# Kernel optimization log

Measured on AMD Instinct MI355X. Metric: run time of the kernel, lower is better.

## Reference

```python
import jax, jax.numpy as jnp
import numpy as np
import math

B, H, W = 4, 256, 256
S = 256          # num_superpixels
ZD = 128         # z_dim
GC = 256         # g_channels
NBLK = 8


def setup_inputs() -> dict:
    key = jax.random.key(0)
    ks = jax.random.split(key, 12)
    rn = lambda k, shp, s=1.0: jax.random.normal(k, shp, jnp.float32) * s
    return {
        "z": rn(ks[0], (B, ZD)),
        "images": rn(ks[1], (B, 3, H, W)),
        "segments": jax.random.randint(ks[2], (B, H, W), 0, S).astype(jnp.int32),
        # row-stochastic-ish adjacency scale keeps 8 propagations stable
        "A": rn(ks[3], (B, S, S), 1.0 / math.sqrt(S)),
        # WSConv2d weights: init N(0,1); forward multiplies input by sqrt(2/(in*k*k))
        "proj_w": rn(ks[4], (GC, 3 + ZD)), "proj_b": jnp.zeros((GC,), jnp.float32),
        "blk_proj_w": rn(ks[5], (NBLK, GC, GC)), "blk_proj_b": jnp.zeros((NBLK, GC), jnp.float32),
        "ada1_w": rn(ks[6], (NBLK, 2 * GC, GC)), "ada1_b": jnp.zeros((NBLK, 2 * GC), jnp.float32),
        "ada2_w": rn(ks[7], (NBLK, 2 * GC, 2 * GC)), "ada2_b": jnp.zeros((NBLK, 2 * GC), jnp.float32),
        # plain Conv2d 3x3 layers in upsample head
        "up1_w": rn(ks[8], (GC // 2, GC, 3, 3), 0.02), "up1_b": jnp.zeros((GC // 2,), jnp.float32),
        "up2_w": rn(ks[9], (3, GC // 2, 3, 3), 0.02), "up2_b": jnp.zeros((3,), jnp.float32),
    }


def _ws1x1(x, w, b):
    # WSConv2d with 1x1 kernel over node dim: x [B,Cin,S] -> [B,Cout,S]
    scale = math.sqrt(2.0 / w.shape[1])
    return jnp.einsum('oc,bcs->bos', w, x) * scale + b[None, :, None]


def _conv3(x, w, b):
    y = jax.lax.conv_general_dilated(x, w, (1, 1), 'SAME',
                                     dimension_numbers=('NCHW', 'OIHW', 'NCHW'))
    return y + b[None, :, None, None]


def _forward(z, images, A, proj_w, proj_b, blk_proj_w, blk_proj_b,
             ada1_w, ada1_b, ada2_w, ada2_b, up1_w, up1_b, up2_w, up2_b,
             segments):
    Bn, _, Hn, Wn = images.shape
    N = Hn * Wn
    flat = images.reshape(Bn, 3, N)            # [B,3,N]
    seg = segments.reshape(Bn, N)              # [B,N] int

    # superpixel mean pooling (math of one_hot^T @ flat / counts, as segment-sum)
    seg_sum = jax.vmap(lambda f, s: jax.ops.segment_sum(f, s, num_segments=S))(
        flat.transpose(0, 2, 1), seg)          # [B,S,3]
    counts = jax.vmap(lambda s: jax.ops.segment_sum(
        jnp.ones(s.shape, jnp.float32), s, num_segments=S))(seg)  # [B,S]
    feats = seg_sum / (counts[..., None] + 1e-6)

    z_rep = jnp.broadcast_to(z[:, None, :], (Bn, S, ZD))
    x = jnp.concatenate([feats, z_rep], axis=2).transpose(0, 2, 1)  # [B,3+ZD,S]
    x = _ws1x1(x, proj_w, proj_b)                                   # [B,GC,S]

    for i in range(NBLK):
        h = _ws1x1(x, blk_proj_w[i], blk_proj_b[i])
        # A @ feat : out[b,c,i] = sum_j A[b,i,j] h[b,c,j]
        h = jnp.einsum('bij,bcj->bci', A, h)
        # AdaIN: style from global mean over nodes
        m = h.mean(axis=2, keepdims=True)                    # [B,GC,1]
        s1 = jax.nn.leaky_relu(_ws1x1(m, ada1_w[i], ada1_b[i]), 0.2)
        style = _ws1x1(s1, ada2_w[i], ada2_b[i])             # [B,2GC,1]
        gamma, beta = jnp.split(style, 2, axis=1)
        h = gamma * h + beta
        x = jax.nn.leaky_relu(h, 0.2)                        # dropout=0 (eval)

    # broadcast superpixel feats back to pixels (math of one_hot @ sup_feats)
    sup_feats = x.transpose(0, 2, 1)                         # [B,S,GC]
    pix = jnp.take_along_axis(sup_feats, seg[:, :, None].astype(jnp.int32), axis=1)  # [B,N,GC]
    pix = pix.transpose(0, 2, 1).reshape(Bn, GC, Hn, Wn)

    y = jax.nn.leaky_relu(_conv3(pix, up1_w, up1_b), 0.2)
    y = _conv3(y, up2_w, up2_b)                              # [B,3,H,W]
    # InstanceNorm2d(3), affine=False, eps=1e-5
    mu = y.mean((2, 3), keepdims=True)
    var = y.var((2, 3), keepdims=True)
    y = (y - mu) / jnp.sqrt(var + 1e-5)
    return jnp.tanh(y)


def reference(z, images, segments, A, proj_w, proj_b, blk_proj_w, blk_proj_b,
              ada1_w, ada1_b, ada2_w, ada2_b, up1_w, up1_b, up2_w, up2_b):
    return _forward(z, images, A, proj_w, proj_b, blk_proj_w, blk_proj_b,
                    ada1_w, ada1_b, ada2_w, ada2_b, up1_w, up1_b, up2_w, up2_b,
                    segments)
```

## Files before the change

### kernel.cpp

```cpp
#include <hip/hip_runtime.h>
#include <cmath>

#define BB 4
#define SS 256
#define ZDIM 128
#define GCH 256
#define NBLKS 8
#define NPIX 65536
#define U1C 128

__device__ __forceinline__ float lrelu(float x){ return x >= 0.f ? x : 0.2f*x; }

__global__ __launch_bounds__(256) void k_pp(const float* __restrict__ img,
        const int* __restrict__ seg, float* __restrict__ segsum,
        float* __restrict__ counts, const float* __restrict__ A,
        const float* __restrict__ w1, const float* __restrict__ w2,
        float* __restrict__ At2, float* __restrict__ wT, float* __restrict__ w2t){
  int bid = blockIdx.x;
  int tid = threadIdx.x;
  if(bid < 256){
    __shared__ float ls[SS*4];
    for(int j=tid;j<SS*4;j+=256) ls[j]=0.f;
    __syncthreads();
    int b = bid >> 6;
    int base = bid*1024;
    for(int it=0; it<4; it++){
      int idx = base + it*256 + tid;
      int n = idx & (NPIX-1);
      int s = seg[idx];
      atomicAdd(&ls[s*4+0], img[(b*3+0)*NPIX+n]);
      atomicAdd(&ls[s*4+1], img[(b*3+1)*NPIX+n]);
      atomicAdd(&ls[s*4+2], img[(b*3+2)*NPIX+n]);
      atomicAdd(&ls[s*4+3], 1.0f);
    }
    __syncthreads();
    for(int j=tid;j<SS*4;j+=256){
      int s = j>>2, c = j&3;
      float vv = ls[j];
      if(vv != 0.f){
        if(c<3) atomicAdd(&segsum[(b*SS+s)*3+c], vv);
        else    atomicAdd(&counts[b*SS+s], vv);
      }
    }
  } else if(bid < 512){
    __shared__ float t[32][33];
    int sb = bid - 256;
    int b = sb >> 6;
    int bx = (sb & 7)*32, by = ((sb >> 3) & 7)*32;
    int lx = tid & 31, ly4 = (tid >> 5)*4;
    #pragma unroll
    for(int r=0;r<4;r++)
      t[ly4+r][lx] = A[(b<<16) + ((by+ly4+r)<<8) + bx + lx];
    __syncthreads();
    #pragma unroll
    for(int r=0;r<4;r++){
      int jj = bx + ly4 + r;
      int i  = by + lx;
      At2[(b<<16) + ((jj>>2)<<10) + (i<<2) + (jj&3)] = t[lx][ly4+r];
    }
  } else {
    int idx = (bid-512)*256 + tid;
    if(idx < 294912){
      int o = idx & 127; int r = idx >> 7; int c = r & 255; int k = r >> 8;
      wT[idx] = w1[(o*GCH + c)*9 + k];
    } else if(idx < 294912 + 3456){
      int t2 = idx - 294912;
      int cc = t2 & 7;
      int oc = (t2 >> 3) % 3;
      int sg = (t2 / 24) & 3;
      int g  = (t2 / 96) & 3;
      int k  = t2 / 384;
      w2t[t2] = w2[oc*1152 + (g*32 + sg*8 + cc)*9 + k];
    }
  }
}

__global__ __launch_bounds__(256) void k_x0(const float* __restrict__ segsum,
        const float* __restrict__ counts, const float* __restrict__ z,
        const float* __restrict__ pw, const float* __restrict__ pb,
        float sc, float4* __restrict__ xp2){
  int og = blockIdx.x;
  int b  = blockIdx.y;
  int i  = threadIdx.x;
  float cnt = counts[b*SS+i] + 1e-6f;
  float f0 = segsum[(b*SS+i)*3+0]/cnt;
  float f1 = segsum[(b*SS+i)*3+1]/cnt;
  float f2 = segsum[(b*SS+i)*3+2]/cnt;
  const float* zb = z + b*ZDIM;
  float vals[4];
  #pragma unroll
  for(int oo=0;oo<4;oo++){
    int o = og*4 + oo;
    const float* wr = pw + o*131;
    float acc = wr[0]*f0 + wr[1]*f1 + wr[2]*f2;
    #pragma unroll 8
    for(int j=0;j<ZDIM;j++) acc += wr[3+j]*zb[j];
    vals[oo] = acc*sc + pb[o];
  }
  float4 o4 = {vals[0], vals[1], vals[2], vals[3]};
  xp2[(b*64+og)*256 + i] = o4;
}

__global__ __launch_bounds__(512) void k_gemm(const float4* __restrict__ xp2,
        const float* __restrict__ bw, const float* __restrict__ bb,
        const float4* __restrict__ At2, float sc,
        float* __restrict__ h2, float* __restrict__ m){
  int c0 = blockIdx.x*4;
  int b  = blockIdx.y;
  int tid = threadIdx.x;
  int j  = tid & 255;
  int h  = tid >> 8;
  __shared__ float4 wl4[4][64];
  __shared__ float ps[8][260];
  __shared__ float4 h1l4[4][66];
  __shared__ float red[4][4];
  for(int t = tid; t < 1024; t += 512){
    int row = t >> 8, jj = t & 255;
    ((float*)&wl4[row][0])[jj] = bw[(c0+row)*GCH + jj];
  }
  __syncthreads();
  {
    const float4* xb = xp2 + (b*64 + h*32)*256 + j;
    float a0=0.f, a1=0.f, a2=0.f, a3=0.f;
    #pragma unroll 8
    for(int kg=0; kg<32; kg++){
      float4 x  = xb[kg*256];
      float4 w0 = wl4[0][h*32+kg];
      float4 w1v= wl4[1][h*32+kg];
      float4 w2v= wl4[2][h*32+kg];
      float4 w3 = wl4[3][h*32+kg];
      a0 += w0.x*x.x + w0.y*x.y + w0.z*x.z + w0.w*x.w;
      a1 += w1v.x*x.x + w1v.y*x.y + w1v.z*x.z + w1v.w*x.w;
      a2 += w2v.x*x.x + w2v.y*x.y + w2v.z*x.z + w2v.w*x.w;
      a3 += w3.x*x.x + w3.y*x.y + w3.z*x.z + w3.w*x.w;
    }
    ps[0+h][j] = a0; ps[2+h][j] = a1; ps[4+h][j] = a2; ps[6+h][j] = a3;
  }
  __syncthreads();
  if(tid < 256){
    #pragma unroll
    for(int ch=0;ch<4;ch++){
      float vv = (ps[ch*2][tid] + ps[ch*2+1][tid])*sc + bb[c0+ch];
      ((float*)&h1l4[ch][0])[tid] = vv;
    }
  }
  __syncthreads();
  {
    const float4* ab = At2 + (b*64 + h*32)*256 + j;
    float r0=0.f, r1=0.f, r2=0.f, r3=0.f;
    #pragma unroll 8
    for(int kg=0; kg<32; kg++){
      float4 a  = ab[kg*256];
      float4 h0 = h1l4[0][h*32+kg];
      float4 h1 = h1l4[1][h*32+kg];
      float4 h2v= h1l4[2][h*32+kg];
      float4 h3 = h1l4[3][h*32+kg];
      r0 += a.x*h0.x + a.y*h0.y + a.z*h0.z + a.w*h0.w;
      r1 += a.x*h1.x + a.y*h1.y + a.z*h1.z + a.w*h1.w;
      r2 += a.x*h2v.x + a.y*h2v.y + a.z*h2v.z + a.w*h2v.w;
      r3 += a.x*h3.x + a.y*h3.y + a.z*h3.z + a.w*h3.w;
    }
    ps[0+h][j] = r0; ps[2+h][j] = r1; ps[4+h][j] = r2; ps[6+h][j] = r3;
  }
  __syncthreads();
  float rr0=0.f, rr1=0.f, rr2=0.f, rr3=0.f;
  if(tid < 256){
    rr0 = ps[0][tid]+ps[1][tid];
    rr1 = ps[2][tid]+ps[3][tid];
    rr2 = ps[4][tid]+ps[5][tid];
    rr3 = ps[6][tid]+ps[7][tid];
    h2[(b*GCH+c0+0)*SS + tid] = rr0;
    h2[(b*GCH+c0+1)*SS + tid] = rr1;
    h2[(b*GCH+c0+2)*SS + tid] = rr2;
    h2[(b*GCH+c0+3)*SS + tid] = rr3;
  }
  for(int off=32; off; off>>=1){
    rr0 += __shfl_down(rr0,off); rr1 += __shfl_down(rr1,off);
    rr2 += __shfl_down(rr2,off); rr3 += __shfl_down(rr3,off);
  }
  if(tid < 256 && (tid & 63)==0){
    int w3 = tid >> 6;
    red[0][w3]=rr0; red[1][w3]=rr1; red[2][w3]=rr2; red[3][w3]=rr3;
  }
  __syncthreads();
  if(tid < 4)
    m[b*GCH + c0 + tid] =
      (red[tid][0]+red[tid][1]+red[tid][2]+red[tid][3])*(1.f/256.f);
}

__global__ __launch_bounds__(512) void k_s12(const float* __restrict__ m,
        const float* __restrict__ a1w, const float* __restrict__ a1b,
        const float* __restrict__ a2w, const float* __restrict__ a2b,
        const float* __restrict__ h2, float sc1, float sc2,
        float4* __restrict__ xp2){
  int q = blockIdx.x;
  int tid = threadIdx.x;
  int lane = tid & 63, wv = tid >> 6;
  int grp = lane >> 3, ll = lane & 7;
  __shared__ float4 ml4[256];
  __shared__ float s1l[4][512];
  __shared__ float gbl[4][16];
  if(tid < 256) ml4[tid] = ((const float4*)m)[tid];
  __syncthreads();
  #pragma unroll 2
  for(int pass=0; pass<8; pass++){
    int row = wv*64 + pass*8 + grp;
    const float4* ar = (const float4*)(a1w + row*GCH) + ll;
    float p0=0.f,p1=0.f,p2=0.f,p3=0.f;
    #pragma unroll
    for(int j=0;j<8;j++){
      float4 w4 = ar[j*8];
      float4 m0 = ml4[0*64 + j*8 + ll];
      float4 m1 = ml4[1*64 + j*8 + ll];
      float4 m2 = ml4[2*64 + j*8 + ll];
      float4 m3 = ml4[3*64 + j*8 + ll];
      p0 += w4.x*m0.x + w4.y*m0.y + w4.z*m0.z + w4.w*m0.w;
      p1 += w4.x*m1.x + w4.y*m1.y + w4.z*m1.z + w4.w*m1.w;
      p2 += w4.x*m2.x + w4.y*m2.y + w4.z*m2.z + w4.w*m2.w;
      p3 += w4.x*m3.x + w4.y*m3.y + w4.z*m3.z + w4.w*m3.w;
    }
    #pragma unroll
    for(int off=1; off<8; off<<=1){
      p0 += __shfl_xor(p0,off); p1 += __shfl_xor(p1,off);
      p2 += __shfl_xor(p2,off); p3 += __shfl_xor(p3,off);
    }
    if(ll == 0){
      float bv = a1b[row];
      int sidx = ((row & 7) << 6) + (row >> 3);
      s1l[0][sidx] = lrelu(p0*sc1 + bv);
      s1l[1][sidx] = lrelu(p1*sc1 + bv);
      s1l[2][sidx] = lrelu(p2*sc1 + bv);
      s1l[3][sidx] = lrelu(p3*sc1 + bv);
    }
  }
  __syncthreads();
  float sA[4][8];
  #pragma unroll
  for(int b=0;b<4;b++)
    #pragma unroll
    for(int j=0;j<8;j++) sA[b][j] = s1l[b][j*64 + lane];
  #pragma unroll
  for(int r=0;r<2;r++){
    int ridx = wv*2 + r;
    int cc = ridx & 7;
    int t = (ridx < 8) ? (q*8 + cc) : (256 + q*8 + cc);
    const float* wr = a2w + t*512 + lane*8;
    float4 wa = *(const float4*)wr;
    float4 wb4 = *(const float4*)(wr+4);
    float p0 = wa.x*sA[0][0]+wa.y*sA[0][1]+wa.z*sA[0][2]+wa.w*sA[0][3]
             + wb4.x*sA[0][4]+wb4.y*sA[0][5]+wb4.z*sA[0][6]+wb4.w*sA[0][7];
    float p1 = wa.x*sA[1][0]+wa.y*sA[1][1]+wa.z*sA[1][2]+wa.w*sA[1][3]
             + wb4.x*sA[1][4]+wb4.y*sA[1][5]+wb4.z*sA[1][6]+wb4.w*sA[1][7];
    float p2 = wa.x*sA[2][0]+wa.y*sA[2][1]+wa.z*sA[2][2]+wa.w*sA[2][3]
             + wb4.x*sA[2][4]+wb4.y*sA[2][5]+wb4.z*sA[2][6]+wb4.w*sA[2][7];
    float p3 = wa.x*sA[3][0]+wa.y*sA[3][1]+wa.z*sA[3][2]+wa.w*sA[3][3]
             + wb4.x*sA[3][4]+wb4.y*sA[3][5]+wb4.z*sA[3][6]+wb4.w*sA[3][7];
    for(int off=32; off; off>>=1){
      p0 += __shfl_xor(p0,off); p1 += __shfl_xor(p1,off);
      p2 += __shfl_xor(p2,off); p3 += __shfl_xor(p3,off);
    }
    if(lane < 4){
      float p = lane==0 ? p0 : lane==1 ? p1 : lane==2 ? p2 : p3;
      gbl[lane][ridx] = p*sc2 + a2b[t];
    }
  }
  __syncthreads();
  int j = tid & 255;
  int cg2 = tid >> 8;
  int cbase = q*8 + cg2*4;
  int cg = cbase >> 2;
  #pragma unroll
  for(int b=0;b<4;b++){
    float4 o;
    o.x = lrelu(gbl[b][cg2*4+0]*h2[(b*GCH + cbase+0)*SS + j] + gbl[b][8+cg2*4+0]);
    o.y = lrelu(gbl[b][cg2*4+1]*h2[(b*GCH + cbase+1)*SS + j] + gbl[b][8+cg2*4+1]);
    o.z = lrelu(gbl[b][cg2*4+2]*h2[(b*GCH + cbase+2)*SS + j] + gbl[b][8+cg2*4+2]);
    o.w = lrelu(gbl[b][cg2*4+3]*h2[(b*GCH + cbase+3)*SS + j] + gbl[b][8+cg2*4+3]);
    xp2[(b*64 + cg)*256 + j] = o;
  }
}

__global__ __launch_bounds__(256) void k_v(const float4* __restrict__ xp2,
        const float4* __restrict__ wT4, float4* __restrict__ v4){
  int s0 = blockIdx.x*16;
  int k  = blockIdx.y;
  int b  = blockIdx.z;
  int tid = threadIdx.x;
  __shared__ float4 wl[64][33];
  __shared__ float xft[256][17];
  for(int t = tid; t < 1024; t += 256){
    int cg = t >> 4, si = t & 15;
    float4 xv = xp2[(b*64 + cg)*256 + s0 + si];
    xft[cg*4+0][si] = xv.x;
    xft[cg*4+1][si] = xv.y;
    xft[cg*4+2][si] = xv.z;
    xft[cg*4+3][si] = xv.w;
  }
  int og = tid & 31, sh = tid >> 5;
  const float4* wb = wT4 + (size_t)k*GCH*32;
  float4 a0 = {0.f,0.f,0.f,0.f}, a1 = {0.f,0.f,0.f,0.f};
  for(int ct=0; ct<4; ct++){
    __syncthreads();
    for(int t = tid; t < 2048; t += 256){
      int cc = t>>5, o = t&31;
      wl[cc][o] = wb[(ct*64+cc)*32 + o];
    }
    __syncthreads();
    #pragma unroll 4
    for(int cc=0;cc<64;cc++){
      float4 w = wl[cc][og];
      int c = ct*64+cc;
      float x0v = xft[c][sh];
      float x1v = xft[c][8+sh];
      a0.x += w.x*x0v; a0.y += w.y*x0v; a0.z += w.z*x0v; a0.w += w.w*x0v;
      a1.x += w.x*x1v; a1.y += w.y*x1v; a1.z += w.z*x1v; a1.w += w.w*x1v;
    }
  }
  size_t base = (size_t)(b*9+k)*SS + s0;
  v4[(base + sh)*32 + og]     = a0;
  v4[(base + 8 + sh)*32 + og] = a1;
}

__global__ __launch_bounds__(256) void k_conv(const float4* __restrict__ v4,
        const int* __restrict__ seg, const float4* __restrict__ b14,
        const float* __restrict__ w2t, float* __restrict__ y2){
  __shared__ float4 y1t4[100*9];
  __shared__ int   segl[144];
  __shared__ float part[768];
  int bid = blockIdx.x;
  int x = bid & 7;
  int b = x >> 1;
  int sub = ((bid >> 3) << 1) + (x & 1);
  int g = sub & 3;
  int tile = sub >> 2;
  int x0p = (tile & 31)*8, y0p = (tile >> 5)*8;
  int tid = threadIdx.x;
  if(tid < 144){
    int r = tid/12, cc = tid%12;
    int gy = y0p - 2 + r, gx = x0p - 2 + cc;
    segl[tid] = (gy>=0 && gy<256 && gx>=0 && gx<256) ? seg[(b*256+gy)*256+gx] : -1;
  }
  __syncthreads();
  int o2 = tid & 3;
  const float4* vb = v4 + (size_t)(b*9)*SS*32 + g*8 + o2*2;
  float4 biasA = b14[g*8 + o2*2];
  float4 biasB = b14[g*8 + o2*2 + 1];
  bool interior = (x0p >= 8 && x0p <= 240 && y0p >= 8 && y0p <= 240);
  if(interior){
    for(int task = tid; task < 400; task += 256){
      int pp = task >> 2;
      int py = pp/10, px = pp - py*10;
      float4 aA = biasA, aB = biasB;
      #pragma unroll
      for(int k=0;k<9;k++){
        int sidx = segl[(py + k/3)*12 + (px + k%3)];
        const float4* pv = vb + (k*SS + sidx)*32;
        float4 vA = pv[0], vB = pv[1];
        aA.x += vA.x; aA.y += vA.y; aA.z += vA.z; aA.w += vA.w;
        aB.x += vB.x; aB.y += vB.y; aB.z += vB.z; aB.w += vB.w;
      }
      float4 valA, valB;
      valA.x = lrelu(aA.x); valA.y = lrelu(aA.y); valA.z = lrelu(aA.z); valA.w = lrelu(aA.w);
      valB.x = lrelu(aB.x); valB.y = lrelu(aB.y); valB.z = lrelu(aB.z); valB.w = lrelu(aB.w);
      y1t4[pp*9 + o2*2]     = valA;
      y1t4[pp*9 + o2*2 + 1] = valB;
    }
  } else {
    for(int task = tid; task < 400; task += 256){
      int pp = task >> 2;
      int py = pp/10, px = pp - py*10;
      int gy = y0p - 1 + py, gx = x0p - 1 + px;
      bool pix_ok = (gy>=0 && gy<256 && gx>=0 && gx<256);
      float4 aA = biasA, aB = biasB;
      #pragma unroll
      for(int k=0;k<9;k++){
        int sidx = segl[(py + k/3)*12 + (px + k%3)];
        int sidx0 = sidx < 0 ? 0 : sidx;
        float msk = sidx < 0 ? 0.f : 1.f;
        const float4* pv = vb + (k*SS + sidx0)*32;
        float4 vA = pv[0], vB = pv[1];
        aA.x += msk*vA.x; aA.y += msk*vA.y; aA.z += msk*vA.z; aA.w += msk*vA.w;
        aB.x += msk*vB.x; aB.y += msk*vB.y; aB.z += msk*vB.z; aB.w += msk*vB.w;
      }
      float4 valA, valB;
      valA.x = pix_ok ? lrelu(aA.x) : 0.f;
      valA.y = pix_ok ? lrelu(aA.y) : 0.f;
      valA.z = pix_ok ? lrelu(aA.z) : 0.f;
      valA.w = pix_ok ? lrelu(aA.w) : 0.f;
      valB.x = pix_ok ? lrelu(aB.x) : 0.f;
      valB.y = pix_ok ? lrelu(aB.y) : 0.f;
      valB.z = pix_ok ? lrelu(aB.z) : 0.f;
      valB.w = pix_ok ? lrelu(aB.w) : 0.f;
      y1t4[pp*9 + o2*2]     = valA;
      y1t4[pp*9 + o2*2 + 1] = valB;
    }
  }
  __syncthreads();
  int pxo = tid & 63, sg = tid >> 6;
  int sgu = __builtin_amdgcn_readfirstlane(sg);
  const float* wk0 = w2t + (g*4 + sgu)*24;
  int ty = pxo >> 3, tx = pxo & 7;
  float p0=0.f,p1=0.f,p2=0.f;
  #pragma unroll
  for(int k=0;k<9;k++){
    int pp0 = (ty + k/3)*10 + (tx + k%3);
    float4 ya = y1t4[pp0*9 + sgu*2];
    float4 yb = y1t4[pp0*9 + sgu*2 + 1];
    const float* wk = wk0 + k*384;
    p0 += wk[0]*ya.x + wk[1]*ya.y + wk[2]*ya.z + wk[3]*ya.w
        + wk[4]*yb.x + wk[5]*yb.y + wk[6]*yb.z + wk[7]*yb.w;
    p1 += wk[8]*ya.x + wk[9]*ya.y + wk[10]*ya.z + wk[11]*ya.w
        + wk[12]*yb.x + wk[13]*yb.y + wk[14]*yb.z + wk[15]*yb.w;
    p2 += wk[16]*ya.x + wk[17]*ya.y + wk[18]*ya.z + wk[19]*ya.w
        + wk[20]*yb.x + wk[21]*yb.y + wk[22]*yb.z + wk[23]*yb.w;
  }
  part[tid]     = p0;
  part[256+tid] = p1;
  part[512+tid] = p2;
  __syncthreads();
  if(tid < 64){
    float s0 = part[tid]    +part[tid+64]    +part[tid+128]    +part[tid+192];
    float s1 = part[256+tid]+part[256+tid+64]+part[256+tid+128]+part[256+tid+192];
    float s2 = part[512+tid]+part[512+tid+64]+part[512+tid+128]+part[512+tid+192];
    int gy = y0p + (tid>>3), gx = x0p + (tid&7);
    int nidx = gy*256+gx;
    atomicAdd(&y2[(b*3+0)*NPIX+nidx], s0);
    atomicAdd(&y2[(b*3+1)*NPIX+nidx], s1);
    atomicAdd(&y2[(b*3+2)*NPIX+nidx], s2);
  }
}

__global__ void k_stats(const float* __restrict__ y2, double* __restrict__ stats){
  int bc = blockIdx.x;
  int chunk = blockIdx.y;
  const float* p = y2 + (size_t)bc*NPIX + chunk*8192;
  int t = threadIdx.x;
  double s=0.0, q=0.0;
  for(int i=t;i<8192;i+=256){ double vv = (double)p[i]; s+=vv; q+=vv*vv; }
  __shared__ double rs[256], rq[256];
  rs[t]=s; rq[t]=q; __syncthreads();
  for(int st=128; st; st>>=1){ if(t<st){rs[t]+=rs[t+st]; rq[t]+=rq[t+st];} __syncthreads(); }
  if(t==0){ atomicAdd(&stats[bc*2], rs[0]); atomicAdd(&stats[bc*2+1], rq[0]); }
}

__global__ void k_norm(const float* __restrict__ y2, const double* __restrict__ stats,
                       float* __restrict__ out){
  int bu = (blockIdx.x*256) >> 16;
  double mu  = stats[bu*2+0] * (1.0/65536.0);
  double ex2 = stats[bu*2+1] * (1.0/65536.0);
  double var = ex2 - mu*mu;
  float inv = (float)(1.0/sqrt(var + 1e-5));
  float mf = (float)mu;
  int idx = blockIdx.x*256+threadIdx.x;
  out[idx] = tanhf((y2[idx]-mf)*inv);
}

extern "C" void kernel_launch(void* const* d_in, const int* in_sizes, int n_in,
                              void* d_out, int out_size, void* d_ws, size_t ws_size,
                              hipStream_t stream) {
  const float* z   = (const float*)d_in[0];
  const float* img = (const float*)d_in[1];
  const int*   seg = (const int*)d_in[2];
  const float* A   = (const float*)d_in[3];
  const float* pw  = (const float*)d_in[4];
  const float* pb  = (const float*)d_in[5];
  const float* bw  = (const float*)d_in[6];
  const float* bb  = (const float*)d_in[7];
  const float* a1w = (const float*)d_in[8];
  const float* a1b = (const float*)d_in[9];
  const float* a2w = (const float*)d_in[10];
  const float* a2b = (const float*)d_in[11];
  const float* w1  = (const float*)d_in[12];
  const float* b1  = (const float*)d_in[13];
  const float* w2  = (const float*)d_in[14];
  const float* b2  = (const float*)d_in[15]; (void)b2;
  float* out = (float*)d_out;

  float* ws = (float*)d_ws;
  float* segsum = ws;
  float* counts = ws + 3072;
  float* m      = ws + 4096;
  double* stats = (double*)(ws + 5120);
  float* xp2 = ws + 5248;
  float* h2  = xp2 + 262144;
  float* At2 = h2 + 262144;
  float* wT  = At2 + 262144;
  float* v   = wT + 294912;
  float* y2  = v + 1179648;
  float* w2t = y2 + 786432;

  hipMemsetAsync(ws, 0, 5248*sizeof(float), stream);
  hipMemsetAsync(y2, 0, 786432*sizeof(float), stream);

  float sProj = (float)sqrt(2.0/131.0);
  float s256  = (float)sqrt(2.0/256.0);
  float s512  = (float)sqrt(2.0/512.0);

  k_pp  <<<512 + 1166, 256, 0, stream>>>(img, seg, segsum, counts,
                                         A, w1, w2, At2, wT, w2t);
  k_x0  <<<dim3(64,4), 256, 0, stream>>>(segsum, counts, z, pw, pb, sProj,
                                         (float4*)xp2);

  for(int blk=0; blk<NBLKS; blk++){
    k_gemm<<<dim3(64,4), 512, 0, stream>>>((const float4*)xp2,
                                           bw + blk*GCH*GCH, bb + blk*GCH,
                                           (const float4*)At2, s256, h2, m);
    k_s12 <<<32, 512, 0, stream>>>(m, a1w + blk*512*GCH, a1b + blk*512,
                                   a2w + blk*512*512, a2b + blk*512,
                                   h2, s256, s512, (float4*)xp2);
  }

  k_v   <<<dim3(16,9,4), 256, 0, stream>>>((const float4*)xp2, (const float4*)wT,
                                           (float4*)v);
  k_conv<<<16384, 256, 0, stream>>>((const float4*)v, seg, (const float4*)b1, w2t, y2);
  k_stats<<<dim3(12,8), 256, 0, stream>>>(y2, stats);
  k_norm<<<3072, 256, 0, stream>>>(y2, stats, out);
}
```

Before: 371.3 us.

## Fuse AdaIN modulation into next GEMM prologue and enlarge conv tiles

The gamma/beta modulation and leaky ReLU that k_s12 used to apply to h2 are moved into the next k_gemm's input load and into k_v. k_s12 now only writes the style vectors, and h2 is ping-ponged between two buffers stored in packed float4 layout. This removes one full read-write pass over h2 per block. Separately, k_conv tiles grow from 8x8 to 16x8 pixels with two channel subgroups of 16 instead of four of 8, which halves the block count and the halo overhead but uses more shared memory per block.

```diff
diff --git a/kernel.cpp b/kernel.cpp
--- a/kernel.cpp
+++ b/kernel.cpp
@@ -65,12 +65,12 @@
       wT[idx] = w1[(o*GCH + c)*9 + k];
     } else if(idx < 294912 + 3456){
       int t2 = idx - 294912;
-      int cc = t2 & 7;
-      int oc = (t2 >> 3) % 3;
-      int sg = (t2 / 24) & 3;
+      int cc = t2 & 15;
+      int oc = (t2 >> 4) % 3;
+      int sg = (t2 / 48) & 1;
       int g  = (t2 / 96) & 3;
       int k  = t2 / 384;
-      w2t[t2] = w2[oc*1152 + (g*32 + sg*8 + cc)*9 + k];
+      w2t[t2] = w2[oc*1152 + (g*32 + sg*16 + cc)*9 + k];
     }
   }
 }
@@ -101,16 +101,18 @@
   xp2[(b*64+og)*256 + i] = o4;
 }
 
-__global__ __launch_bounds__(512) void k_gemm(const float4* __restrict__ xp2,
+__global__ __launch_bounds__(512) void k_gemm(const float4* __restrict__ h2prev,
+        const float* __restrict__ gbPrev,
         const float* __restrict__ bw, const float* __restrict__ bb,
         const float4* __restrict__ At2, float sc,
-        float* __restrict__ h2, float* __restrict__ m){
+        float4* __restrict__ h2next, float* __restrict__ m){
   int c0 = blockIdx.x*4;
   int b  = blockIdx.y;
   int tid = threadIdx.x;
   int j  = tid & 255;
   int h  = tid >> 8;
   __shared__ float4 wl4[4][64];
+  __shared__ float4 glG4[128];
   __shared__ float ps[8][260];
   __shared__ float4 h1l4[4][66];
   __shared__ float red[4][4];
@@ -118,21 +120,45 @@
     int row = t >> 8, jj = t & 255;
     ((float*)&wl4[row][0])[jj] = bw[(c0+row)*GCH + jj];
   }
+  if(gbPrev) ((float*)glG4)[tid] = gbPrev[b*512 + tid];
   __syncthreads();
   {
-    const float4* xb = xp2 + (b*64 + h*32)*256 + j;
+    const float4* xb = h2prev + (size_t)(b*64 + h*32)*256 + j;
     float a0=0.f, a1=0.f, a2=0.f, a3=0.f;
-    #pragma unroll 8
-    for(int kg=0; kg<32; kg++){
-      float4 x  = xb[kg*256];
-      float4 w0 = wl4[0][h*32+kg];
-      float4 w1v= wl4[1][h*32+kg];
-      float4 w2v= wl4[2][h*32+kg];
-      float4 w3 = wl4[3][h*32+kg];
-      a0 += w0.x*x.x + w0.y*x.y + w0.z*x.z + w0.w*x.w;
-      a1 += w1v.x*x.x + w1v.y*x.y + w1v.z*x.z + w1v.w*x.w;
-      a2 += w2v.x*x.x + w2v.y*x.y + w2v.z*x.z + w2v.w*x.w;
-      a3 += w3.x*x.x + w3.y*x.y + w3.z*x.z + w3.w*x.w;
+    if(gbPrev){
+      #pragma unroll 8
+      for(int kg=0; kg<32; kg++){
+        float4 x = xb[kg*256];
+        int kga = h*32 + kg;
+        float4 g4 = glG4[kga];
+        float4 t4 = glG4[64 + kga];
+        x.x = lrelu(g4.x*x.x + t4.x);
+        x.y = lrelu(g4.y*x.y + t4.y);
+        x.z = lrelu(g4.z*x.z + t4.z);
+        x.w = lrelu(g4.w*x.w + t4.w);
+        float4 w0 = wl4[0][kga];
+        float4 w1v= wl4[1][kga];
+        float4 w2v= wl4[2][kga];
+        float4 w3 = wl4[3][kga];
+        a0 += w0.x*x.x + w0.y*x.y + w0.z*x.z + w0.w*x.w;
+        a1 += w1v.x*x.x + w1v.y*x.y + w1v.z*x.z + w1v.w*x.w;
+        a2 += w2v.x*x.x + w2v.y*x.y + w2v.z*x.z + w2v.w*x.w;
+        a3 += w3.x*x.x + w3.y*x.y + w3.z*x.z + w3.w*x.w;
+      }
+    } else {
+      #pragma unroll 8
+      for(int kg=0; kg<32; kg++){
+        float4 x = xb[kg*256];
+        int kga = h*32 + kg;
+        float4 w0 = wl4[0][kga];
+        float4 w1v= wl4[1][kga];
+        float4 w2v= wl4[2][kga];
+        float4 w3 = wl4[3][kga];
+        a0 += w0.x*x.x + w0.y*x.y + w0.z*x.z + w0.w*x.w;
+        a1 += w1v.x*x.x + w1v.y*x.y + w1v.z*x.z + w1v.w*x.w;
+        a2 += w2v.x*x.x + w2v.y*x.y + w2v.z*x.z + w2v.w*x.w;
+        a3 += w3.x*x.x + w3.y*x.y + w3.z*x.z + w3.w*x.w;
+      }
     }
     ps[0+h][j] = a0; ps[2+h][j] = a1; ps[4+h][j] = a2; ps[6+h][j] = a3;
   }
@@ -146,7 +172,7 @@
   }
   __syncthreads();
   {
-    const float4* ab = At2 + (b*64 + h*32)*256 + j;
+    const float4* ab = At2 + (size_t)(b*64 + h*32)*256 + j;
     float r0=0.f, r1=0.f, r2=0.f, r3=0.f;
     #pragma unroll 8
     for(int kg=0; kg<32; kg++){
@@ -169,10 +195,8 @@
     rr1 = ps[2][tid]+ps[3][tid];
     rr2 = ps[4][tid]+ps[5][tid];
     rr3 = ps[6][tid]+ps[7][tid];
-    h2[(b*GCH+c0+0)*SS + tid] = rr0;
-    h2[(b*GCH+c0+1)*SS + tid] = rr1;
-    h2[(b*GCH+c0+2)*SS + tid] = rr2;
-    h2[(b*GCH+c0+3)*SS + tid] = rr3;
+    float4 o; o.x = rr0; o.y = rr1; o.z = rr2; o.w = rr3;
+    h2next[(size_t)(b*64 + (c0>>2))*256 + tid] = o;
   }
   for(int off=32; off; off>>=1){
     rr0 += __shfl_down(rr0,off); rr1 += __shfl_down(rr1,off);
@@ -191,15 +215,13 @@
 __global__ __launch_bounds__(512) void k_s12(const float* __restrict__ m,
         const float* __restrict__ a1w, const float* __restrict__ a1b,
         const float* __restrict__ a2w, const float* __restrict__ a2b,
-        const float* __restrict__ h2, float sc1, float sc2,
-        float4* __restrict__ xp2){
+        float sc1, float sc2, float* __restrict__ gbNext){
   int q = blockIdx.x;
   int tid = threadIdx.x;
   int lane = tid & 63, wv = tid >> 6;
   int grp = lane >> 3, ll = lane & 7;
   __shared__ float4 ml4[256];
   __shared__ float s1l[4][512];
-  __shared__ float gbl[4][16];
   if(tid < 256) ml4[tid] = ((const float4*)m)[tid];
   __syncthreads();
   #pragma unroll 2
@@ -261,40 +283,33 @@
     }
     if(lane < 4){
       float p = lane==0 ? p0 : lane==1 ? p1 : lane==2 ? p2 : p3;
-      gbl[lane][ridx] = p*sc2 + a2b[t];
-    }
-  }
-  __syncthreads();
-  int j = tid & 255;
-  int cg2 = tid >> 8;
-  int cbase = q*8 + cg2*4;
-  int cg = cbase >> 2;
-  #pragma unroll
-  for(int b=0;b<4;b++){
-    float4 o;
-    o.x = lrelu(gbl[b][cg2*4+0]*h2[(b*GCH + cbase+0)*SS + j] + gbl[b][8+cg2*4+0]);
-    o.y = lrelu(gbl[b][cg2*4+1]*h2[(b*GCH + cbase+1)*SS + j] + gbl[b][8+cg2*4+1]);
-    o.z = lrelu(gbl[b][cg2*4+2]*h2[(b*GCH + cbase+2)*SS + j] + gbl[b][8+cg2*4+2]);
-    o.w = lrelu(gbl[b][cg2*4+3]*h2[(b*GCH + cbase+3)*SS + j] + gbl[b][8+cg2*4+3]);
-    xp2[(b*64 + cg)*256 + j] = o;
-  }
-}
-
-__global__ __launch_bounds__(256) void k_v(const float4* __restrict__ xp2,
+      gbNext[lane*512 + t] = p*sc2 + a2b[t];
+    }
+  }
+}
+
+__global__ __launch_bounds__(256) void k_v(const float4* __restrict__ h2f,
+        const float* __restrict__ gbF,
         const float4* __restrict__ wT4, float4* __restrict__ v4){
   int s0 = blockIdx.x*16;
   int k  = blockIdx.y;
   int b  = blockIdx.z;
   int tid = threadIdx.x;
+  __shared__ float4 glV4[128];
   __shared__ float4 wl[64][33];
   __shared__ float xft[256][17];
+  ((float*)glV4)[tid] = gbF[b*512 + tid];
+  ((float*)glV4)[256+tid] = gbF[b*512 + 256 + tid];
+  __syncthreads();
   for(int t = tid; t < 1024; t += 256){
     int cg = t >> 4, si = t & 15;
-    float4 xv = xp2[(b*64 + cg)*256 + s0 + si];
-    xft[cg*4+0][si] = xv.x;
-    xft[cg*4+1][si] = xv.y;
-    xft[cg*4+2][si] = xv.z;
-    xft[cg*4+3][si] = xv.w;
+    float4 xv = h2f[(size_t)(b*64 + cg)*256 + s0 + si];
+    float4 g4 = glV4[cg];
+    float4 t4 = glV4[64 + cg];
+    xft[cg*4+0][si] = lrelu(g4.x*xv.x + t4.x);
+    xft[cg*4+1][si] = lrelu(g4.y*xv.y + t4.y);
+    xft[cg*4+2][si] = lrelu(g4.z*xv.z + t4.z);
+    xft[cg*4+3][si] = lrelu(g4.w*xv.w + t4.w);
   }
   int og = tid & 31, sh = tid >> 5;
   const float4* wb = wT4 + (size_t)k*GCH*32;
@@ -324,8 +339,8 @@
 __global__ __launch_bounds__(256) void k_conv(const float4* __restrict__ v4,
         const int* __restrict__ seg, const float4* __restrict__ b14,
         const float* __restrict__ w2t, float* __restrict__ y2){
-  __shared__ float4 y1t4[100*9];
-  __shared__ int   segl[144];
+  __shared__ float4 y1t4[180*9];
+  __shared__ int   segl[240];
   __shared__ float part[768];
   int bid = blockIdx.x;
   int x = bid & 7;
@@ -333,10 +348,10 @@
   int sub = ((bid >> 3) << 1) + (x & 1);
   int g = sub & 3;
   int tile = sub >> 2;
-  int x0p = (tile & 31)*8, y0p = (tile >> 5)*8;
+  int x0p = (tile & 15)*16, y0p = (tile >> 4)*8;
   int tid = threadIdx.x;
-  if(tid < 144){
-    int r = tid/12, cc = tid%12;
+  if(tid < 240){
+    int r = tid/20, cc = tid%20;
     int gy = y0p - 2 + r, gx = x0p - 2 + cc;
     segl[tid] = (gy>=0 && gy<256 && gx>=0 && gx<256) ? seg[(b*256+gy)*256+gx] : -1;
   }
@@ -345,15 +360,15 @@
   const float4* vb = v4 + (size_t)(b*9)*SS*32 + g*8 + o2*2;
   float4 biasA = b14[g*8 + o2*2];
   float4 biasB = b14[g*8 + o2*2 + 1];
-  bool interior = (x0p >= 8 && x0p <= 240 && y0p >= 8 && y0p <= 240);
+  bool interior = (x0p >= 16 && x0p <= 224 && y0p >= 8 && y0p <= 240);
   if(interior){
-    for(int task = tid; task < 400; task += 256){
+    for(int task = tid; task < 720; task += 256){
       int pp = task >> 2;
-      int py = pp/10, px = pp - py*10;
+      int py = pp/18, px = pp - py*18;
       float4 aA = biasA, aB = biasB;
       #pragma unroll
       for(int k=0;k<9;k++){
-        int sidx = segl[(py + k/3)*12 + (px + k%3)];
+        int sidx = segl[(py + k/3)*20 + (px + k%3)];
         const float4* pv = vb + (k*SS + sidx)*32;
         float4 vA = pv[0], vB = pv[1];
         aA.x += vA.x; aA.y += vA.y; aA.z += vA.z; aA.w += vA.w;
@@ -366,15 +381,15 @@
       y1t4[pp*9 + o2*2 + 1] = valB;
     }
   } else {
-    for(int task = tid; task < 400; task += 256){
+    for(int task = tid; task < 720; task += 256){
       int pp = task >> 2;
-      int py = pp/10, px = pp - py*10;
+      int py = pp/18, px = pp - py*18;
       int gy = y0p - 1 + py, gx = x0p - 1 + px;
       bool pix_ok = (gy>=0 && gy<256 && gx>=0 && gx<256);
       float4 aA = biasA, aB = biasB;
       #pragma unroll
       for(int k=0;k<9;k++){
-        int sidx = segl[(py + k/3)*12 + (px + k%3)];
+        int sidx = segl[(py + k/3)*20 + (px + k%3)];
         int sidx0 = sidx < 0 ? 0 : sidx;
         float msk = sidx < 0 ? 0.f : 1.f;
         const float4* pv = vb + (k*SS + sidx0)*32;
@@ -396,33 +411,41 @@
     }
   }
   __syncthreads();
-  int pxo = tid & 63, sg = tid >> 6;
+  int pxo = tid & 127, sg = tid >> 7;
   int sgu = __builtin_amdgcn_readfirstlane(sg);
-  const float* wk0 = w2t + (g*4 + sgu)*24;
-  int ty = pxo >> 3, tx = pxo & 7;
+  const float* wk0 = w2t + (g*2 + sgu)*48;
+  int ty = pxo >> 4, tx = pxo & 15;
   float p0=0.f,p1=0.f,p2=0.f;
   #pragma unroll
   for(int k=0;k<9;k++){
-    int pp0 = (ty + k/3)*10 + (tx + k%3);
-    float4 ya = y1t4[pp0*9 + sgu*2];
-    float4 yb = y1t4[pp0*9 + sgu*2 + 1];
+    int pp0 = (ty + k/3)*18 + (tx + k%3);
+    float4 ya = y1t4[pp0*9 + sgu*4 + 0];
+    float4 yb = y1t4[pp0*9 + sgu*4 + 1];
+    float4 yc = y1t4[pp0*9 + sgu*4 + 2];
+    float4 yd = y1t4[pp0*9 + sgu*4 + 3];
     const float* wk = wk0 + k*384;
     p0 += wk[0]*ya.x + wk[1]*ya.y + wk[2]*ya.z + wk[3]*ya.w
-        + wk[4]*yb.x + wk[5]*yb.y + wk[6]*yb.z + wk[7]*yb.w;
-    p1 += wk[8]*ya.x + wk[9]*ya.y + wk[10]*ya.z + wk[11]*ya.w
-        + wk[12]*yb.x + wk[13]*yb.y + wk[14]*yb.z + wk[15]*yb.w;
-    p2 += wk[16]*ya.x + wk[17]*ya.y + wk[18]*ya.z + wk[19]*ya.w
-        + wk[20]*yb.x + wk[21]*yb.y + wk[22]*yb.z + wk[23]*yb.w;
+        + wk[4]*yb.x + wk[5]*yb.y + wk[6]*yb.z + wk[7]*yb.w
+        + wk[8]*yc.x + wk[9]*yc.y + wk[10]*yc.z + wk[11]*yc.w
+        + wk[12]*yd.x + wk[13]*yd.y + wk[14]*yd.z + wk[15]*yd.w;
+    p1 += wk[16]*ya.x + wk[17]*ya.y + wk[18]*ya.z + wk[19]*ya.w
+        + wk[20]*yb.x + wk[21]*yb.y + wk[22]*yb.z + wk[23]*yb.w
+        + wk[24]*yc.x + wk[25]*yc.y + wk[26]*yc.z + wk[27]*yc.w
+        + wk[28]*yd.x + wk[29]*yd.y + wk[30]*yd.z + wk[31]*yd.w;
+    p2 += wk[32]*ya.x + wk[33]*ya.y + wk[34]*ya.z + wk[35]*ya.w
+        + wk[36]*yb.x + wk[37]*yb.y + wk[38]*yb.z + wk[39]*yb.w
+        + wk[40]*yc.x + wk[41]*yc.y + wk[42]*yc.z + wk[43]*yc.w
+        + wk[44]*yd.x + wk[45]*yd.y + wk[46]*yd.z + wk[47]*yd.w;
   }
   part[tid]     = p0;
   part[256+tid] = p1;
   part[512+tid] = p2;
   __syncthreads();
-  if(tid < 64){
-    float s0 = part[tid]    +part[tid+64]    +part[tid+128]    +part[tid+192];
-    float s1 = part[256+tid]+part[256+tid+64]+part[256+tid+128]+part[256+tid+192];
-    float s2 = part[512+tid]+part[512+tid+64]+part[512+tid+128]+part[512+tid+192];
-    int gy = y0p + (tid>>3), gx = x0p + (tid&7);
+  if(tid < 128){
+    float s0 = part[tid]     + part[tid+128];
+    float s1 = part[256+tid] + part[256+tid+128];
+    float s2 = part[512+tid] + part[512+tid+128];
+    int gy = y0p + (tid>>4), gx = x0p + (tid&15);
     int nidx = gy*256+gx;
     atomicAdd(&y2[(b*3+0)*NPIX+nidx], s0);
     atomicAdd(&y2[(b*3+1)*NPIX+nidx], s1);
@@ -481,9 +504,11 @@
   float* counts = ws + 3072;
   float* m      = ws + 4096;
   double* stats = (double*)(ws + 5120);
-  float* xp2 = ws + 5248;
-  float* h2  = xp2 + 262144;
-  float* At2 = h2 + 262144;
+  float* gb0 = ws + 5248;
+  float* gb1 = gb0 + 2048;
+  float* h2a = ws + 9344;
+  float* h2b = h2a + 262144;
+  float* At2 = h2b + 262144;
   float* wT  = At2 + 262144;
   float* v   = wT + 294912;
   float* y2  = v + 1179648;
@@ -499,20 +524,26 @@
   k_pp  <<<512 + 1166, 256, 0, stream>>>(img, seg, segsum, counts,
                                          A, w1, w2, At2, wT, w2t);
   k_x0  <<<dim3(64,4), 256, 0, stream>>>(segsum, counts, z, pw, pb, sProj,
-                                         (float4*)xp2);
+                                         (float4*)h2a);
 
   for(int blk=0; blk<NBLKS; blk++){
-    k_gemm<<<dim3(64,4), 512, 0, stream>>>((const float4*)xp2,
+    const float* h2p = (blk & 1) ? h2b : h2a;
+    float*       h2n = (blk & 1) ? h2a : h2b;
+    const float* gbp = (blk == 0) ? (const float*)nullptr
+                                  : ((blk & 1) ? gb0 : gb1);
+    float*       gbn = (blk & 1) ? gb1 : gb0;
+    k_gemm<<<dim3(64,4), 512, 0, stream>>>((const float4*)h2p, gbp,
                                            bw + blk*GCH*GCH, bb + blk*GCH,
-                                           (const float4*)At2, s256, h2, m);
+                                           (const float4*)At2, s256,
+                                           (float4*)h2n, m);
     k_s12 <<<32, 512, 0, stream>>>(m, a1w + blk*512*GCH, a1b + blk*512,
                                    a2w + blk*512*512, a2b + blk*512,
-                                   h2, s256, s512, (float4*)xp2);
-  }
-
-  k_v   <<<dim3(16,9,4), 256, 0, stream>>>((const float4*)xp2, (const float4*)wT,
-                                           (float4*)v);
-  k_conv<<<16384, 256, 0, stream>>>((const float4*)v, seg, (const float4*)b1, w2t, y2);
+                                   s256, s512, gbn);
+  }
+
+  k_v   <<<dim3(16,9,4), 256, 0, stream>>>((const float4*)h2a, gb1,
+                                           (const float4*)wT, (float4*)v);
+  k_conv<<<8192, 256, 0, stream>>>((const float4*)v, seg, (const float4*)b1, w2t, y2);
   k_stats<<<dim3(12,8), 256, 0, stream>>>(y2, stats);
   k_norm<<<3072, 256, 0, stream>>>(y2, stats, out);
 }
```

Measured after the change: 370.8 us. No clear change (-0.1%).
